# Kernel tuning notes

Hardware: AMD Instinct MI355X
Metric: run time of the kernel (lower is better)

The kernel has to match this reference:

```python
import jax, jax.numpy as jnp
import numpy as np

N_NODES = 524288
N_EDGES = 786432
NUM_GRAPHS = 8192
NUM_NODE_TYPES = 16
NODE_DIM = 256
EDGE_DIM = 128
OUT_DIM = 1


def setup_inputs() -> dict:
    key = jax.random.key(0)
    ks = jax.random.split(key, 12)
    h_node = jax.random.uniform(ks[0], (N_NODES, NUM_NODE_TYPES), dtype=jnp.float32)
    pos_node = jax.random.normal(ks[1], (N_NODES, 3), dtype=jnp.float32)
    batch_node = jnp.sort(jax.random.randint(ks[2], (N_NODES,), 0, NUM_GRAPHS)).astype(jnp.int64)
    edge_index = jax.random.randint(ks[3], (2, N_EDGES), 0, N_NODES).astype(jnp.int64)
    batch_edge = jnp.sort(jax.random.randint(ks[4], (N_EDGES,), 0, NUM_GRAPHS)).astype(jnp.int64)
    s = 0.05
    W_node = jax.random.normal(ks[5], (NUM_NODE_TYPES, NODE_DIM), dtype=jnp.float32) * s
    W_edge = jax.random.normal(ks[6], (2 * NUM_NODE_TYPES, EDGE_DIM), dtype=jnp.float32) * s
    H = NODE_DIM + EDGE_DIM
    W1 = jax.random.normal(ks[7], (H, H), dtype=jnp.float32) * s
    b1 = jnp.zeros((H,), dtype=jnp.float32)
    W2 = jax.random.normal(ks[8], (H, OUT_DIM), dtype=jnp.float32) * s
    b2 = jnp.zeros((OUT_DIM,), dtype=jnp.float32)
    return {"h_node": h_node, "pos_node": pos_node, "batch_node": batch_node,
            "edge_index": edge_index, "batch_edge": batch_edge,
            "W_node": W_node, "W_edge": W_edge, "W1": W1, "b1": b1, "W2": W2, "b2": b2}


def _segment_mean(x, seg_ids, num_segments):
    # fused replacement for the original per-graph boolean-mask loop:
    # h[seg==k].mean(0) for all k, via one scatter-add + count normalize
    sums = jax.ops.segment_sum(x, seg_ids, num_segments=num_segments)
    cnts = jax.ops.segment_sum(jnp.ones((x.shape[0],), x.dtype), seg_ids, num_segments=num_segments)
    return sums / jnp.maximum(cnts, 1.0)[:, None]


def reference(h_node, pos_node, batch_node, edge_index, batch_edge,
              W_node, W_edge, W1, b1, W2, b2):
    # h_edge = cat(h_node[src], h_node[dst])  -> [E, 2*num_node_types]
    h_edge_raw = jnp.concatenate([h_node[edge_index[0]], h_node[edge_index[1]]], axis=-1)
    # num_timesteps == 0 path: plain embedders, no time embedding
    hn = h_node @ W_node          # [N, node_dim]
    he = h_edge_raw @ W_edge      # [E, edge_dim]
    # encoder treated as identity (NodeEdgeNet not in scope); pooling is the target op
    node_mean = _segment_mean(hn, batch_node, NUM_GRAPHS)  # [G, node_dim]
    edge_mean = _segment_mean(he, batch_edge, NUM_GRAPHS)  # [G, edge_dim]
    h_sub = jnp.concatenate([node_mean, edge_mean], axis=-1)  # [G, node_dim+edge_dim]
    # final MLP (num_layer=2): Linear -> ReLU -> Linear
    pred = jax.nn.relu(h_sub @ W1 + b1) @ W2 + b2  # [G, 1]
    return pred
```

## Files before the change

### kernel.cpp

```cpp
#include <hip/hip_runtime.h>

#define N_NODES_C   524288
#define N_EDGES_C   786432
#define NUM_GRAPHS_C 8192
#define NT 16
#define NODE_DIM_C 256
#define EDGE_DIM_C 128
#define HDIM 384
#define KC 48

#define FOLD_BLOCKS 72
#define NODE_BLOCKS 2048
#define EDGE_BLOCKS 16384
#define NODE_BASE   FOLD_BLOCKS
#define EDGE_BASE   (FOLD_BLOCKS + NODE_BLOCKS)
#define TOTAL_BLOCKS (FOLD_BLOCKS + NODE_BLOCKS + EDGE_BLOCKS)

#define WS_NM    0
#define WS_EM8   524288
#define WS_WC    8912896
#define WS_ES    8986624
#define WS_NS    9019456
#define WS_BOFF  9052288
#define WS_REC   9576576

__device__ __forceinline__ void f4_add(float4& a, const float4 v) {
    a.x += v.x; a.y += v.y; a.z += v.z; a.w += v.w;
}

__device__ __forceinline__ void f4_shfl_xor_add(float4& a, int mask) {
    a.x += __shfl_xor(a.x, mask, 64);
    a.y += __shfl_xor(a.y, mask, 64);
    a.z += __shfl_xor(a.z, mask, 64);
    a.w += __shfl_xor(a.w, mask, 64);
}

__global__ __launch_bounds__(256) void k0_prep(
    const int* __restrict__ bnode, const int* __restrict__ bedge,
    int* __restrict__ estart, int* __restrict__ nstart) {
    int i = blockIdx.x * 256 + threadIdx.x;
    if (i < N_EDGES_C) {
        int g0 = bedge[i];
        int hi = (i + 1 < N_EDGES_C) ? bedge[i + 1] : NUM_GRAPHS_C;
        if (i == 0) for (int g = 0; g <= g0; ++g) estart[g] = 0;
        for (int g = g0 + 1; g <= hi; ++g) estart[g] = i + 1;
    }
    if (i < N_NODES_C) {
        int g0 = bnode[i];
        int hi = (i + 1 < N_NODES_C) ? bnode[i + 1] : NUM_GRAPHS_C;
        if (i == 0) for (int g = 0; g <= g0; ++g) nstart[g] = 0;
        for (int g = g0 + 1; g <= hi; ++g) nstart[g] = i + 1;
    }
}

__global__ __launch_bounds__(256) void kr_build(
    const int* __restrict__ esrc, const int* __restrict__ edst,
    const int* __restrict__ estart,
    int* __restrict__ rec, int* __restrict__ binoff) {
    int wave = threadIdx.x >> 6, lane = threadIdx.x & 63;
    int g = blockIdx.x * 4 + wave;
    int s = estart[g], e = estart[g + 1];
    __shared__ int lcnt[4][16];
    __shared__ int lcur[4][16];
    if (lane < 16) lcnt[wave][lane] = 0;
    for (int i = s + lane; i < e; i += 64) {
        int a = esrc[i];
        atomicAdd(&lcnt[wave][((a >> 16) << 1) + 0], 1);
        int b = edst[i];
        atomicAdd(&lcnt[wave][((b >> 16) << 1) + 1], 1);
    }
    int c = (lane < 16) ? lcnt[wave][lane] : 0;
    int incl = c;
    #pragma unroll
    for (int d = 1; d < 16; d <<= 1) {
        int v = __shfl_up(incl, d, 64);
        if (lane >= d) incl += v;
    }
    int excl = incl - c;
    if (lane < 16) {
        lcur[wave][lane] = excl;
        binoff[g * 16 + lane] = 2 * s + excl;
    }
    for (int i = s + lane; i < e; i += 64) {
        int a = esrc[i];
        int pa = atomicAdd(&lcur[wave][((a >> 16) << 1) + 0], 1);
        rec[2 * s + pa] = a;
        int b = edst[i];
        int pb = atomicAdd(&lcur[wave][((b >> 16) << 1) + 1], 1);
        rec[2 * s + pb] = b;
    }
}

__global__ __launch_bounds__(256) void km_mega(
    const float* __restrict__ h_node,
    const int* __restrict__ estart, const int* __restrict__ nstart,
    const int* __restrict__ binoff, const int* __restrict__ rec,
    const float* __restrict__ Wn, const float* __restrict__ We,
    const float* __restrict__ W1,
    float* __restrict__ nm, float* __restrict__ em8, float* __restrict__ Wc) {
    int blk  = blockIdx.x;
    int wave = threadIdx.x >> 6;
    int lane = threadIdx.x & 63;
    const float4* h4 = (const float4*)h_node;
    const float4 z4 = make_float4(0.f, 0.f, 0.f, 0.f);

    if (blk < FOLD_BLOCKS) {
        int o = blk * 256 + threadIdx.x;
        if (o >= KC * HDIM) return;
        int k = o / HDIM, j = o % HDIM;
        float acc = 0.f;
        if (k < NT) {
            const float* wr = &Wn[k * NODE_DIM_C];
            #pragma unroll 16
            for (int kk = 0; kk < NODE_DIM_C; ++kk)
                acc = fmaf(wr[kk], W1[(size_t)kk * HDIM + j], acc);
        } else {
            const float* wr = &We[(k - NT) * EDGE_DIM_C];
            #pragma unroll 16
            for (int kk = 0; kk < EDGE_DIM_C; ++kk)
                acc = fmaf(wr[kk], W1[(size_t)(NODE_DIM_C + kk) * HDIM + j], acc);
        }
        Wc[o] = acc;
    } else if (blk < EDGE_BASE) {
        int r = blk - NODE_BASE;
        int s8 = r & 7;
        int g  = s8 * 1024 + (r >> 3) * 4 + wave;
        int s = nstart[g], e = nstart[g + 1];
        int row_off = lane >> 2;
        int quad    = lane & 3;
        float4 a0 = z4, a1 = z4;
        int i = s + row_off;
        for (; i + 16 < e; i += 32) {
            float4 v0 = h4[(size_t)i * 4 + quad];
            float4 v1 = h4[(size_t)(i + 16) * 4 + quad];
            f4_add(a0, v0);
            f4_add(a1, v1);
        }
        if (i < e) f4_add(a0, h4[(size_t)i * 4 + quad]);
        f4_add(a0, a1);
        f4_shfl_xor_add(a0, 4);
        f4_shfl_xor_add(a0, 8);
        f4_shfl_xor_add(a0, 16);
        f4_shfl_xor_add(a0, 32);
        if (row_off == 0) {
            float inv = 1.f / fmaxf((float)(e - s), 1.f);
            ((float4*)nm)[(size_t)g * 4 + quad] =
                make_float4(a0.x * inv, a0.y * inv, a0.z * inv, a0.w * inv);
        }
    } else {
        int r     = blk - EDGE_BASE;
        int slice = r & 7;
        int g     = (r >> 3) * 4 + wave;
        int base0 = binoff[g * 16 + slice * 2];
        int base1 = binoff[g * 16 + slice * 2 + 1];
        int end1  = (slice == 7) ? 2 * estart[g + 1]
                                 : binoff[g * 16 + slice * 2 + 2];
        int slot = lane >> 3;
        int p    = (lane >> 2) & 1;
        int quad = lane & 3;
        int st = p ? base1 : base0;
        int en = p ? end1  : base1;
        int cmax = max(base1 - base0, end1 - base1);
        int T = (cmax + 7) >> 3;
        float4 acc = z4;
        int i = st + slot;
        int idx = (i < en) ? rec[i] : -1;
        for (int t = 1; t < T; ++t) {
            int i2 = i + 8;
            int nx = (i2 < en) ? rec[i2] : -1;
            if (idx >= 0) f4_add(acc, h4[(size_t)idx * 4 + quad]);
            idx = nx; i = i2;
        }
        if (idx >= 0) f4_add(acc, h4[(size_t)idx * 4 + quad]);
        f4_shfl_xor_add(acc, 8);
        f4_shfl_xor_add(acc, 16);
        f4_shfl_xor_add(acc, 32);
        if (slot == 0) {
            ((float4*)em8)[((size_t)(slice * NUM_GRAPHS_C + g)) * 8 + p * 4 + quad] = acc;
        }
    }
}

#define GPB 16
__global__ __launch_bounds__(HDIM) void k3_mlp(
    const float* __restrict__ nm, const float* __restrict__ em8,
    const int* __restrict__ estart,
    const float* __restrict__ Wc, const float* __restrict__ b1,
    const float* __restrict__ W2, const float* __restrict__ b2,
    float* __restrict__ pred) {
    int j = threadIdx.x;
    float wc[KC];
    #pragma unroll
    for (int k = 0; k < KC; ++k) wc[k] = Wc[k * HDIM + j];
    float b1j = b1[j], w2j = W2[j], b20 = b2[0];

    __shared__ float fs[GPB][KC];
    __shared__ float part[GPB][6];
    int g0 = blockIdx.x * GPB;
    for (int t = j; t < GPB * KC; t += HDIM) {
        int g = t / KC, k = t % KC;
        int G = g0 + g;
        float val;
        if (k < NT) {
            val = nm[(size_t)G * NT + k];
        } else {
            float ssum = 0.f;
            #pragma unroll
            for (int s = 0; s < 8; ++s)
                ssum += em8[((size_t)(s * NUM_GRAPHS_C + G)) * 32 + (k - NT)];
            float ec = (float)(estart[G + 1] - estart[G]);
            val = ssum / fmaxf(ec, 1.f);
        }
        fs[g][k] = val;
    }
    __syncthreads();

    int wave = j >> 6, lane = j & 63;
    for (int g = 0; g < GPB; ++g) {
        float z = b1j;
        #pragma unroll
        for (int k = 0; k < KC; ++k) z = fmaf(fs[g][k], wc[k], z);
        z = fmaxf(z, 0.f);
        float p = z * w2j;
        #pragma unroll
        for (int off = 32; off > 0; off >>= 1) p += __shfl_down(p, off, 64);
        if (lane == 0) part[g][wave] = p;
    }
    __syncthreads();
    if (j < GPB) {
        float sacc = b20;
        #pragma unroll
        for (int w = 0; w < 6; ++w) sacc += part[j][w];
        pred[g0 + j] = sacc;
    }
}

extern "C" void kernel_launch(void* const* d_in, const int* in_sizes, int n_in,
                              void* d_out, int out_size, void* d_ws, size_t ws_size,
                              hipStream_t stream) {
    const float* h_node     = (const float*)d_in[0];
    const int*   batch_node = (const int*)d_in[2];
    const int*   edge_index = (const int*)d_in[3];
    const int*   batch_edge = (const int*)d_in[4];
    const float* W_node     = (const float*)d_in[5];
    const float* W_edge     = (const float*)d_in[6];
    const float* W1         = (const float*)d_in[7];
    const float* b1         = (const float*)d_in[8];
    const float* W2         = (const float*)d_in[9];
    const float* b2         = (const float*)d_in[10];
    float* pred = (float*)d_out;

    char* ws = (char*)d_ws;
    float* nm     = (float*)(ws + WS_NM);
    float* em8    = (float*)(ws + WS_EM8);
    float* Wc     = (float*)(ws + WS_WC);
    int*   estart = (int*)(ws + WS_ES);
    int*   nstart = (int*)(ws + WS_NS);
    int*   binoff = (int*)(ws + WS_BOFF);
    int*   rec    = (int*)(ws + WS_REC);

    const int* esrc = edge_index;
    const int* edst = edge_index + N_EDGES_C;

    k0_prep <<<3072, 256, 0, stream>>>(batch_node, batch_edge, estart, nstart);
    kr_build<<<NUM_GRAPHS_C / 4, 256, 0, stream>>>(esrc, edst, estart, rec, binoff);
    km_mega <<<TOTAL_BLOCKS, 256, 0, stream>>>(
        h_node, estart, nstart, binoff, rec, W_node, W_edge, W1, nm, em8, Wc);
    k3_mlp  <<<NUM_GRAPHS_C / GPB, HDIM, 0, stream>>>(
        nm, em8, estart, Wc, b1, W2, b2, pred);
}
```

Before: 143.7 us.

## Fuse prep into bin build via binary search and atomically reduce edge slices

Removes the separate k0_prep launch. Each wave now finds its graph's edge segment bounds by binary search on batch_edge, and node starts are computed inside kr_build. Edge-slice partial sums are scaled by 1/count and atomically added into a compact per-graph buffer, which replaces the 8-slice em8 staging array and the 8-way reduction in the MLP kernel. This saves one launch and a lot of workspace traffic, at the cost of float atomics with nondeterministic summation order and a dependency on zeroing em inside kr_build.

```diff
diff --git a/kernel.cpp b/kernel.cpp
--- a/kernel.cpp
+++ b/kernel.cpp
@@ -17,12 +17,12 @@
 #define TOTAL_BLOCKS (FOLD_BLOCKS + NODE_BLOCKS + EDGE_BLOCKS)
 
 #define WS_NM    0
-#define WS_EM8   524288
-#define WS_WC    8912896
-#define WS_ES    8986624
-#define WS_NS    9019456
-#define WS_BOFF  9052288
-#define WS_REC   9576576
+#define WS_EM    524288
+#define WS_WC    1572864
+#define WS_NS    1646592
+#define WS_BOFF  1679424
+#define WS_ECNT  2203712
+#define WS_REC   2236480
 
 __device__ __forceinline__ void f4_add(float4& a, const float4 v) {
     a.x += v.x; a.y += v.y; a.z += v.z; a.w += v.w;
@@ -35,38 +35,51 @@
     a.w += __shfl_xor(a.w, mask, 64);
 }
 
-__global__ __launch_bounds__(256) void k0_prep(
+__device__ __forceinline__ int lower_bound_i32(const int* __restrict__ a, int n, int key) {
+    int lo = 0, hi = n;
+    while (lo < hi) {
+        int mid = (lo + hi) >> 1;
+        if (a[mid] < key) lo = mid + 1; else hi = mid;
+    }
+    return lo;
+}
+
+__device__ __forceinline__ void wave_seg_bounds(const int* __restrict__ b, int n,
+                                                int g, int lane, int& s, int& e) {
+    int key = g + ((lane >= 32) ? 1 : 0);
+    int lo = lower_bound_i32(b, n, key);
+    s = __shfl(lo, 0, 64);
+    e = __shfl(lo, 32, 64);
+}
+
+__global__ __launch_bounds__(256) void kr_build(
     const int* __restrict__ bnode, const int* __restrict__ bedge,
-    int* __restrict__ estart, int* __restrict__ nstart) {
-    int i = blockIdx.x * 256 + threadIdx.x;
-    if (i < N_EDGES_C) {
-        int g0 = bedge[i];
-        int hi = (i + 1 < N_EDGES_C) ? bedge[i + 1] : NUM_GRAPHS_C;
-        if (i == 0) for (int g = 0; g <= g0; ++g) estart[g] = 0;
-        for (int g = g0 + 1; g <= hi; ++g) estart[g] = i + 1;
-    }
-    if (i < N_NODES_C) {
+    const int* __restrict__ esrc, const int* __restrict__ edst,
+    int* __restrict__ rec, int* __restrict__ binoff,
+    int* __restrict__ ecnt, int* __restrict__ nstart, float* __restrict__ em) {
+    int tid = threadIdx.x, blk = blockIdx.x;
+    int i = blk * 256 + tid;
+    {
         int g0 = bnode[i];
         int hi = (i + 1 < N_NODES_C) ? bnode[i + 1] : NUM_GRAPHS_C;
         if (i == 0) for (int g = 0; g <= g0; ++g) nstart[g] = 0;
         for (int g = g0 + 1; g <= hi; ++g) nstart[g] = i + 1;
     }
-}
-
-__global__ __launch_bounds__(256) void kr_build(
-    const int* __restrict__ esrc, const int* __restrict__ edst,
-    const int* __restrict__ estart,
-    int* __restrict__ rec, int* __restrict__ binoff) {
-    int wave = threadIdx.x >> 6, lane = threadIdx.x & 63;
-    int g = blockIdx.x * 4 + wave;
-    int s = estart[g], e = estart[g + 1];
+    if (tid < 128) em[blk * 128 + tid] = 0.f;
+
+    int wave = tid >> 6, lane = tid & 63;
+    int g = blk * 4 + wave;
+    int s, e;
+    wave_seg_bounds(bedge, N_EDGES_C, g, lane, s, e);
+    if (lane == 0) ecnt[g] = e - s;
+
     __shared__ int lcnt[4][16];
     __shared__ int lcur[4][16];
     if (lane < 16) lcnt[wave][lane] = 0;
-    for (int i = s + lane; i < e; i += 64) {
-        int a = esrc[i];
+    for (int q = s + lane; q < e; q += 64) {
+        int a = esrc[q];
         atomicAdd(&lcnt[wave][((a >> 16) << 1) + 0], 1);
-        int b = edst[i];
+        int b = edst[q];
         atomicAdd(&lcnt[wave][((b >> 16) << 1) + 1], 1);
     }
     int c = (lane < 16) ? lcnt[wave][lane] : 0;
@@ -81,11 +94,11 @@
         lcur[wave][lane] = excl;
         binoff[g * 16 + lane] = 2 * s + excl;
     }
-    for (int i = s + lane; i < e; i += 64) {
-        int a = esrc[i];
+    for (int q = s + lane; q < e; q += 64) {
+        int a = esrc[q];
         int pa = atomicAdd(&lcur[wave][((a >> 16) << 1) + 0], 1);
         rec[2 * s + pa] = a;
-        int b = edst[i];
+        int b = edst[q];
         int pb = atomicAdd(&lcur[wave][((b >> 16) << 1) + 1], 1);
         rec[2 * s + pb] = b;
     }
@@ -93,11 +106,11 @@
 
 __global__ __launch_bounds__(256) void km_mega(
     const float* __restrict__ h_node,
-    const int* __restrict__ estart, const int* __restrict__ nstart,
-    const int* __restrict__ binoff, const int* __restrict__ rec,
+    const int* __restrict__ nstart, const int* __restrict__ binoff,
+    const int* __restrict__ ecnt, const int* __restrict__ rec,
     const float* __restrict__ Wn, const float* __restrict__ We,
     const float* __restrict__ W1,
-    float* __restrict__ nm, float* __restrict__ em8, float* __restrict__ Wc) {
+    float* __restrict__ nm, float* __restrict__ em, float* __restrict__ Wc) {
     int blk  = blockIdx.x;
     int wave = threadIdx.x >> 6;
     int lane = threadIdx.x & 63;
@@ -151,10 +164,11 @@
         int r     = blk - EDGE_BASE;
         int slice = r & 7;
         int g     = (r >> 3) * 4 + wave;
-        int base0 = binoff[g * 16 + slice * 2];
-        int base1 = binoff[g * 16 + slice * 2 + 1];
-        int end1  = (slice == 7) ? 2 * estart[g + 1]
-                                 : binoff[g * 16 + slice * 2 + 2];
+        int b16   = g * 16 + slice * 2;
+        int base0 = binoff[b16];
+        int base1 = binoff[b16 + 1];
+        int cnt   = ecnt[g];
+        int end1  = (slice == 7) ? binoff[g * 16] + 2 * cnt : binoff[b16 + 2];
         int slot = lane >> 3;
         int p    = (lane >> 2) & 1;
         int quad = lane & 3;
@@ -176,15 +190,19 @@
         f4_shfl_xor_add(acc, 16);
         f4_shfl_xor_add(acc, 32);
         if (slot == 0) {
-            ((float4*)em8)[((size_t)(slice * NUM_GRAPHS_C + g)) * 8 + p * 4 + quad] = acc;
+            float inv = 1.f / fmaxf((float)cnt, 1.f);
+            float* dst = &em[(size_t)g * 32 + p * 16 + quad * 4];
+            atomicAdd(dst + 0, acc.x * inv);
+            atomicAdd(dst + 1, acc.y * inv);
+            atomicAdd(dst + 2, acc.z * inv);
+            atomicAdd(dst + 3, acc.w * inv);
         }
     }
 }
 
 #define GPB 16
 __global__ __launch_bounds__(HDIM) void k3_mlp(
-    const float* __restrict__ nm, const float* __restrict__ em8,
-    const int* __restrict__ estart,
+    const float* __restrict__ nm, const float* __restrict__ em,
     const float* __restrict__ Wc, const float* __restrict__ b1,
     const float* __restrict__ W2, const float* __restrict__ b2,
     float* __restrict__ pred) {
@@ -197,21 +215,11 @@
     __shared__ float fs[GPB][KC];
     __shared__ float part[GPB][6];
     int g0 = blockIdx.x * GPB;
+    #pragma unroll
     for (int t = j; t < GPB * KC; t += HDIM) {
         int g = t / KC, k = t % KC;
-        int G = g0 + g;
-        float val;
-        if (k < NT) {
-            val = nm[(size_t)G * NT + k];
-        } else {
-            float ssum = 0.f;
-            #pragma unroll
-            for (int s = 0; s < 8; ++s)
-                ssum += em8[((size_t)(s * NUM_GRAPHS_C + G)) * 32 + (k - NT)];
-            float ec = (float)(estart[G + 1] - estart[G]);
-            val = ssum / fmaxf(ec, 1.f);
-        }
-        fs[g][k] = val;
+        fs[g][k] = (k < NT) ? nm[(size_t)(g0 + g) * NT + k]
+                            : em[(size_t)(g0 + g) * 32 + (k - NT)];
     }
     __syncthreads();
 
@@ -252,20 +260,20 @@
 
     char* ws = (char*)d_ws;
     float* nm     = (float*)(ws + WS_NM);
-    float* em8    = (float*)(ws + WS_EM8);
+    float* em     = (float*)(ws + WS_EM);
     float* Wc     = (float*)(ws + WS_WC);
-    int*   estart = (int*)(ws + WS_ES);
     int*   nstart = (int*)(ws + WS_NS);
     int*   binoff = (int*)(ws + WS_BOFF);
+    int*   ecnt   = (int*)(ws + WS_ECNT);
     int*   rec    = (int*)(ws + WS_REC);
 
     const int* esrc = edge_index;
     const int* edst = edge_index + N_EDGES_C;
 
-    k0_prep <<<3072, 256, 0, stream>>>(batch_node, batch_edge, estart, nstart);
-    kr_build<<<NUM_GRAPHS_C / 4, 256, 0, stream>>>(esrc, edst, estart, rec, binoff);
+    kr_build<<<NUM_GRAPHS_C / 4, 256, 0, stream>>>(
+        batch_node, batch_edge, esrc, edst, rec, binoff, ecnt, nstart, em);
     km_mega <<<TOTAL_BLOCKS, 256, 0, stream>>>(
-        h_node, estart, nstart, binoff, rec, W_node, W_edge, W1, nm, em8, Wc);
+        h_node, nstart, binoff, ecnt, rec, W_node, W_edge, W1, nm, em, Wc);
     k3_mlp  <<<NUM_GRAPHS_C / GPB, HDIM, 0, stream>>>(
-        nm, em8, estart, Wc, b1, W2, b2, pred);
-}
+        nm, em, Wc, b1, W2, b2, pred);
+}
```

Result: slower. 154.5 us (+7.5%).
